# Optimization experiments

Measured on AMD Instinct MI355X. Metric: run time of the kernel, lower is better.

## Reference

```python
import jax, jax.numpy as jnp
import numpy as np

B, C, H, W = 4, 256, 64, 64
CQ = C // 8


def setup_inputs() -> dict:
    key = jax.random.key(0)
    ks = jax.random.split(key, 7)
    x = jax.random.normal(ks[0], (B, C, H, W), dtype=jnp.float32)
    Wq = jax.random.normal(ks[1], (CQ, C), dtype=jnp.float32) * 0.02
    bq = jnp.zeros((CQ,), dtype=jnp.float32)
    Wk = jax.random.normal(ks[2], (CQ, C), dtype=jnp.float32) * 0.02
    bk = jnp.zeros((CQ,), dtype=jnp.float32)
    Wv = jax.random.normal(ks[3], (C, C), dtype=jnp.float32) * 0.02
    bv = jnp.zeros((C,), dtype=jnp.float32)
    return {"x": x, "Wq": Wq, "bq": bq, "Wk": Wk, "bk": bk, "Wv": Wv, "bv": bv}


def reference(x, Wq, bq, Wk, bk, Wv, bv):
    b, c, h, w = x.shape
    n = h * w
    xf = x.reshape(b, c, n)                                   # [B,C,N]
    # 1x1 convs are per-pixel GEMMs
    q = jnp.einsum('qc,bcn->bnq', Wq, xf) + bq                # [B,N,Cq]
    k = jnp.einsum('qc,bcn->bqn', Wk, xf) + bk[None, :, None] # [B,Cq,N]
    v = jnp.einsum('vc,bcn->bnv', Wv, xf) + bv                # [B,N,C]
    scale = float(n) ** 0.5
    energy = jnp.einsum('bnq,bqm->bnm', q, k) / scale         # [B,N,N]
    attn = jax.nn.softmax(energy, axis=-1)
    out = jnp.einsum('bnm,bmv->bnv', attn, v)                 # [B,N,C]
    # Faithful to torch's out.view(B,C,H,W) applied to the contiguous [B,N,C]
    # tensor: a raw memory reinterpretation, NOT a transpose.
    return out.reshape(b, c, h, w)
```

## Files before the change

### kernel.cpp

```cpp
#include <hip/hip_runtime.h>

#define BATCH 4
#define CH    256
#define NPIX  4096
#define CQD   32

typedef __bf16 bf16;
typedef bf16 bf16x8 __attribute__((ext_vector_type(8)));
typedef bf16 bf16x4 __attribute__((ext_vector_type(4)));
typedef float f32x4 __attribute__((ext_vector_type(4)));
typedef float f32x16 __attribute__((ext_vector_type(16)));

#define MFMA16 __builtin_amdgcn_mfma_f32_16x16x32_bf16
#define MFMA32 __builtin_amdgcn_mfma_f32_32x32x16_bf16

#define GLOAD_LDS16(g, l) __builtin_amdgcn_global_load_lds( \
    (const __attribute__((address_space(1))) void*)(g),     \
    (__attribute__((address_space(3))) void*)(l), 16, 0, 0)

__device__ __forceinline__ float fast_exp2(float x) {
#if __has_builtin(__builtin_amdgcn_exp2f)
    return __builtin_amdgcn_exp2f(x);
#else
    return __expf(x * 0.69314718055994530942f);
#endif
}

#define QSCALE (0.015625f * 1.44269504088896340736f)

__global__ __launch_bounds__(256) void prep_kernel(
    const float* __restrict__ Wq, const float* __restrict__ bq,
    const float* __restrict__ Wk, const float* __restrict__ bk,
    const float* __restrict__ Wv, const float* __restrict__ bv,
    bf16* __restrict__ Wb, float* __restrict__ bb)
{
    int r = blockIdx.x, c = threadIdx.x;
    const float* W; const float* bs; float sc; int rr;
    if (r < 32)      { W = Wq; bs = bq; sc = QSCALE; rr = r; }
    else if (r < 64) { W = Wk; bs = bk; sc = 1.0f;   rr = r - 32; }
    else             { W = Wv; bs = bv; sc = 1.0f;   rr = r - 64; }
    Wb[(size_t)r * CH + c] = (bf16)(W[(size_t)rr * CH + c] * sc);
    if (c == 0) bb[r] = bs[rr] * sc;
}

__global__ __launch_bounds__(256) void proj_kernel(
    const float* __restrict__ x,
    const bf16* __restrict__ Wb, const float* __restrict__ bb,
    bf16* __restrict__ qp, bf16* __restrict__ kp, bf16* __restrict__ vT)
{
    __shared__ __align__(16) bf16 xT[32][264];
    __shared__ __align__(16) bf16 vstage[4][16][40];

    const int t  = threadIdx.x;
    const int b  = blockIdx.x >> 7;
    const int n0 = (blockIdx.x & 127) << 5;
    const int w    = t >> 6;
    const int lane = t & 63;
    const int l16  = t & 15;
    const int quad = (t & 63) >> 4;

    const float* xb = x + (size_t)b * CH * NPIX;
#pragma unroll
    for (int j = 0; j < 8; ++j) {
        int id = t + j * 256;
        int c  = id >> 3;
        int n4 = (id & 7) << 2;
        float4 vv = *(const float4*)(xb + (size_t)c * NPIX + n0 + n4);
        xT[n4 + 0][c] = (bf16)vv.x;
        xT[n4 + 1][c] = (bf16)vv.y;
        xT[n4 + 2][c] = (bf16)vv.z;
        xT[n4 + 3][c] = (bf16)vv.w;
    }
    __syncthreads();

    for (int rt = 0; rt < 5; ++rt) {
        int ro = w * 80 + rt * 16;
        int kind = (ro < 32) ? 0 : (ro < 64) ? 1 : 2;

        bf16x8 afrag[8];
        const bf16* wrow = Wb + (size_t)(ro + l16) * CH + quad * 8;
#pragma unroll
        for (int kc = 0; kc < 8; ++kc)
            afrag[kc] = *(const bf16x8*)(wrow + kc * 32);
        float bv4[4];
#pragma unroll
        for (int r = 0; r < 4; ++r) bv4[r] = bb[ro + quad * 4 + r];

#pragma unroll
        for (int nt = 0; nt < 2; ++nt) {
            f32x4 acc = {0.f, 0.f, 0.f, 0.f};
#pragma unroll
            for (int kc = 0; kc < 8; ++kc) {
                bf16x8 bfr = *(const bf16x8*)&xT[nt * 16 + l16][kc * 32 + quad * 8];
                acc = MFMA16(afrag[kc], bfr, acc, 0, 0, 0);
            }
            if (kind != 2) {
                bf16x4 pk;
#pragma unroll
                for (int r = 0; r < 4; ++r)
                    pk[r] = (bf16)(acc[r] + bv4[r]);
                int n = n0 + nt * 16 + l16;
                int col = (kind == 0 ? ro : ro - 32) + quad * 4;
                bf16* dst = (kind == 0) ? qp : kp;
                *(bf16x4*)&dst[((size_t)b * NPIX + n) * CQD + col] = pk;
            } else {
#pragma unroll
                for (int r = 0; r < 4; ++r)
                    vstage[w][quad * 4 + r][nt * 16 + l16] = (bf16)(acc[r] + bv4[r]);
            }
        }
        if (kind == 2) {
            int vrow = lane >> 2, vcc = lane & 3;
            bf16x8 chunk = *(const bf16x8*)&vstage[w][vrow][vcc * 8];
            *(bf16x8*)&vT[((size_t)b * CH + (ro - 64) + vrow) * NPIX + n0 + vcc * 8] = chunk;
        }
    }
}

template<int S, bool DIRECT>
__global__ __launch_bounds__(256, 2) void attn_kernel(
    const bf16* __restrict__ qp, const bf16* __restrict__ kp,
    const bf16* __restrict__ vT,
    bf16* __restrict__ Opart, float* __restrict__ Lpart,
    float* __restrict__ out)
{
    __shared__ __align__(16) bf16 Vt[2][256][64];
    __shared__ __align__(16) bf16 PbS[128][64];

    const int t    = threadIdx.x;
    const int bid  = blockIdx.x;
    const int s    = bid % S;
    const int tq   = bid / S;
    const int b    = tq >> 5;
    const int qt   = tq & 31;
    const int n0   = qt << 7;
    const int w    = t >> 6;
    const int lane = t & 63;
    const int l16  = t & 15;
    const int quad = (t & 63) >> 4;
    const int sw   = l16 & 7;
    const int l32  = lane & 31;
    const int h    = lane >> 5;
    const int qh   = w >> 1;
    const int chb  = (w & 1) * 128;

    const bf16* qpb = qp + ((size_t)b * NPIX + n0 + w * 32) * CQD;
    bf16x8 qfrag[2];
    qfrag[0] = *(const bf16x8*)(qpb + (size_t)l16 * CQD + quad * 8);
    qfrag[1] = *(const bf16x8*)(qpb + (size_t)(16 + l16) * CQD + quad * 8);

    f32x16 o[2][4];
#pragma unroll
    for (int i = 0; i < 2; ++i)
#pragma unroll
        for (int j = 0; j < 4; ++j)
#pragma unroll
            for (int r = 0; r < 16; ++r) o[i][j][r] = 0.f;
    float lsum[2] = {0.f, 0.f};

    const bf16* kpb = kp + (size_t)b * NPIX * CQD;
    const bf16* vTb = vT + (size_t)b * CH * NPIX;
    const int k0 = s * (NPIX / S);
    const int iters = NPIX / S / 64;

    const int vrow_off = lane >> 3;
    const int vchunk   = (lane & 7) ^ vrow_off;
    auto issue_vt = [&](int buf, int m0) {
#pragma unroll
        for (int j = 0; j < 8; ++j) {
            int rowbase = j * 32 + w * 8;
            const bf16* src = vTb + (size_t)(rowbase + vrow_off) * NPIX + m0 + vchunk * 8;
            GLOAD_LDS16(src, &Vt[buf][rowbase][0]);
        }
    };
    auto load_kf = [&](int m0, bf16x8* kf) {
#pragma unroll
        for (int mt = 0; mt < 4; ++mt)
            kf[mt] = *(const bf16x8*)(kpb + (size_t)(m0 + mt * 16 + l16) * CQD + quad * 8);
    };

    bf16x8 kfa[4], kfb[4];
    issue_vt(0, k0);
    load_kf(k0, kfa);
    __syncthreads();

    for (int mi = 0; mi < iters; ++mi) {
        const int cur = mi & 1;
        const int m0  = k0 + (mi << 6);
        if (mi + 1 < iters) {
            issue_vt(cur ^ 1, m0 + 64);
            load_kf(m0 + 64, kfb);
        }

        f32x4 sv[2][4];
#pragma unroll
        for (int mt = 0; mt < 4; ++mt) {
            f32x4 z = {0.f, 0.f, 0.f, 0.f};
            sv[0][mt] = MFMA16(kfa[mt], qfrag[0], z, 0, 0, 0);
            sv[1][mt] = MFMA16(kfa[mt], qfrag[1], z, 0, 0, 0);
        }

#pragma unroll
        for (int g = 0; g < 2; ++g) {
            float rs = 0.f;
#pragma unroll
            for (int mt = 0; mt < 4; ++mt) {
                bf16x4 pk;
#pragma unroll
                for (int r = 0; r < 4; ++r) {
                    float e = fast_exp2(sv[g][mt][r]);
                    rs += e;
                    pk[r] = (bf16)e;
                }
                int slot = (2 * mt + (quad >> 1)) ^ sw;
                *(bf16x4*)&PbS[w * 32 + g * 16 + l16][slot * 8 + (quad & 1) * 4] = pk;
            }
            lsum[g] += rs;
        }
        __syncthreads();

        bf16x8 pA[2][4];
#pragma unroll
        for (int t32 = 0; t32 < 2; ++t32)
#pragma unroll
            for (int kg = 0; kg < 4; ++kg) {
                int row = qh * 64 + t32 * 32 + l32;
                pA[t32][kg] = *(const bf16x8*)&PbS[row][((2 * kg + h) ^ (l32 & 7)) * 8];
            }
#pragma unroll
        for (int ct = 0; ct < 4; ++ct) {
            int vrow = chb + ct * 32 + l32;
            bf16x8 vB[4];
#pragma unroll
            for (int kg = 0; kg < 4; ++kg)
                vB[kg] = *(const bf16x8*)&Vt[cur][vrow][((2 * kg + h) ^ (l32 & 7)) * 8];
#pragma unroll
            for (int t32 = 0; t32 < 2; ++t32)
#pragma unroll
                for (int kg = 0; kg < 4; ++kg)
                    o[t32][ct] = MFMA32(pA[t32][kg], vB[kg], o[t32][ct], 0, 0, 0);
        }
        __syncthreads();
#pragma unroll
        for (int i = 0; i < 4; ++i) kfa[i] = kfb[i];
    }

    float l_g[2];
#pragma unroll
    for (int g = 0; g < 2; ++g) {
        float v = lsum[g];
        v += __shfl_xor(v, 16);
        v += __shfl_xor(v, 32);
        l_g[g] = v;
    }
    float* lsh = (float*)PbS;
    if (quad == 0) {
#pragma unroll
        for (int g = 0; g < 2; ++g)
            lsh[w * 32 + g * 16 + l16] = l_g[g];
    }
    __syncthreads();

    const size_t prb2 = ((size_t)s * BATCH + b) * NPIX + n0;
    if (!DIRECT && quad == 0) {
#pragma unroll
        for (int g = 0; g < 2; ++g)
            Lpart[prb2 + w * 32 + g * 16 + l16] = l_g[g];
    }

    bf16* eb = (bf16*)Vt + (size_t)w * 32 * 136;
#pragma unroll
    for (int t32 = 0; t32 < 2; ++t32) {
        float rinv[16];
#pragma unroll
        for (int reg = 0; reg < 16; ++reg) {
            int q_r = (reg & 3) + 8 * (reg >> 2) + 4 * h;
            rinv[reg] = 1.0f / lsh[qh * 64 + t32 * 32 + q_r];
        }
        if (!DIRECT) {
#pragma unroll
            for (int ct = 0; ct < 4; ++ct)
#pragma unroll
                for (int reg = 0; reg < 16; ++reg) {
                    int q_r = (reg & 3) + 8 * (reg >> 2) + 4 * h;
                    eb[q_r * 136 + ct * 32 + l32] = (bf16)(o[t32][ct][reg] * rinv[reg]);
                }
            int vrow = lane >> 4, vcc = lane & 15;
#pragma unroll
            for (int p = 0; p < 8; ++p) {
                int row = p * 4 + vrow;
                bf16x8 chunk = *(const bf16x8*)&eb[row * 136 + vcc * 8];
                *(bf16x8*)&Opart[(prb2 + qh * 64 + t32 * 32 + row) * CH +
                                 chb + vcc * 8] = chunk;
            }
        } else {
            float* ob = out + (prb2 + qh * 64 + t32 * 32) * CH + chb;
#pragma unroll
            for (int ct = 0; ct < 4; ++ct)
#pragma unroll
                for (int reg = 0; reg < 16; ++reg) {
                    int q_r = (reg & 3) + 8 * (reg >> 2) + 4 * h;
                    ob[(size_t)q_r * CH + ct * 32 + l32] = o[t32][ct][reg] * rinv[reg];
                }
        }
    }
}

template<int S>
__global__ __launch_bounds__(256) void combine_kernel(
    const bf16* __restrict__ Opart, const float* __restrict__ Lpart,
    float* __restrict__ out)
{
    int idx  = blockIdx.x * 256 + threadIdx.x;
    int nrow = idx >> 4;
    int cc   = (idx & 15) * 16;
    int b    = nrow >> 12, nin = nrow & 4095;

    size_t pr[S];
    float  ls[S], wsum = 0.f;
#pragma unroll
    for (int s = 0; s < S; ++s) {
        pr[s] = ((size_t)s * BATCH + b) * NPIX + nin;
        ls[s] = Lpart[pr[s]];
        wsum += ls[s];
    }
    float inv = 1.0f / wsum;

    bf16x8 ov[S][2];
#pragma unroll
    for (int s = 0; s < S; ++s) {
        ov[s][0] = *(const bf16x8*)&Opart[pr[s] * CH + cc];
        ov[s][1] = *(const bf16x8*)&Opart[pr[s] * CH + cc + 8];
    }

    float acc[16];
#pragma unroll
    for (int j = 0; j < 16; ++j) acc[j] = 0.f;
#pragma unroll
    for (int s = 0; s < S; ++s) {
        float wn = ls[s] * inv;
#pragma unroll
        for (int k = 0; k < 2; ++k)
#pragma unroll
            for (int j = 0; j < 8; ++j)
                acc[k * 8 + j] += wn * (float)ov[s][k][j];
    }
#pragma unroll
    for (int k = 0; k < 4; ++k) {
        float4 o4 = {acc[4 * k], acc[4 * k + 1], acc[4 * k + 2], acc[4 * k + 3]};
        *(float4*)&out[(size_t)nrow * CH + cc + 4 * k] = o4;
    }
}

extern "C" void kernel_launch(void* const* d_in, const int* in_sizes, int n_in,
                              void* d_out, int out_size, void* d_ws, size_t ws_size,
                              hipStream_t stream) {
    const float* x  = (const float*)d_in[0];
    const float* Wq = (const float*)d_in[1];
    const float* bq = (const float*)d_in[2];
    const float* Wk = (const float*)d_in[3];
    const float* bk = (const float*)d_in[4];
    const float* Wv = (const float*)d_in[5];
    const float* bv = (const float*)d_in[6];
    float* out = (float*)d_out;

    char* ws = (char*)d_ws;
    const size_t qpB   = (size_t)BATCH * NPIX * CQD * 2;
    const size_t vTB   = (size_t)BATCH * CH * NPIX * 2;
    const size_t WbB   = (size_t)320 * CH * 2;
    const size_t bbB   = 320 * 4 + 768;
    const size_t baseB = 2 * qpB + vTB + WbB + bbB;
    const size_t oprtB = (size_t)BATCH * NPIX * CH * 2;
    const size_t mlB   = (size_t)BATCH * NPIX * 4;

    bf16*  qp = (bf16*)ws;
    bf16*  kp = (bf16*)(ws + qpB);
    bf16*  vT = (bf16*)(ws + 2 * qpB);
    bf16*  Wb = (bf16*)(ws + 2 * qpB + vTB);
    float* bb = (float*)(ws + 2 * qpB + vTB + WbB);

    prep_kernel<<<dim3(320), dim3(256), 0, stream>>>(Wq, bq, Wk, bk, Wv, bv, Wb, bb);
    proj_kernel<<<dim3(BATCH * (NPIX / 32)), dim3(256), 0, stream>>>(
        x, Wb, bb, qp, kp, vT);

    auto need = [&](int S) { return baseB + (size_t)S * (oprtB + mlB); };
    int S = (ws_size >= need(4)) ? 4 : (ws_size >= need(2)) ? 2
          : (ws_size >= need(1)) ? 1 : 0;

    if (S > 0) {
        bf16*  Opart = (bf16*)(ws + baseB);
        float* Lpart = (float*)(ws + baseB + (size_t)S * oprtB);
        if (S == 4) {
            attn_kernel<4, false><<<dim3(128 * 4), dim3(256), 0, stream>>>(
                qp, kp, vT, Opart, Lpart, out);
            combine_kernel<4><<<dim3(1024), dim3(256), 0, stream>>>(Opart, Lpart, out);
        } else if (S == 2) {
            attn_kernel<2, false><<<dim3(128 * 2), dim3(256), 0, stream>>>(
                qp, kp, vT, Opart, Lpart, out);
            combine_kernel<2><<<dim3(1024), dim3(256), 0, stream>>>(Opart, Lpart, out);
        } else {
            attn_kernel<1, false><<<dim3(128), dim3(256), 0, stream>>>(
                qp, kp, vT, Opart, Lpart, out);
            combine_kernel<1><<<dim3(1024), dim3(256), 0, stream>>>(Opart, Lpart, out);
        }
    } else {
        attn_kernel<1, true><<<dim3(128), dim3(256), 0, stream>>>(
            qp, kp, vT, nullptr, nullptr, out);
    }
}
```

Baseline: 142.7 us.

## Give each wave its own query rows for PV to drop block barrier

The PV stage changes so each wave multiplies only its own 32 query rows of P against all 256 value channels. Previously each wave took 64 rows by 128 channels, which read P rows written by other waves. Because each wave now consumes only the P rows it produced, the block-wide barrier between softmax and PV is removed, and the final row-sum exchange uses per-wave LDS with a waitcnt instead of a barrier. In exchange every wave now reads all 256 Vt rows from LDS, doubling V LDS traffic, and holds 8 f32x16 accumulators at the same register count.

```diff
diff --git a/kernel.cpp b/kernel.cpp
--- a/kernel.cpp
+++ b/kernel.cpp
@@ -141,21 +141,17 @@
     const int sw   = l16 & 7;
     const int l32  = lane & 31;
     const int h    = lane >> 5;
-    const int qh   = w >> 1;
-    const int chb  = (w & 1) * 128;
 
     const bf16* qpb = qp + ((size_t)b * NPIX + n0 + w * 32) * CQD;
     bf16x8 qfrag[2];
     qfrag[0] = *(const bf16x8*)(qpb + (size_t)l16 * CQD + quad * 8);
     qfrag[1] = *(const bf16x8*)(qpb + (size_t)(16 + l16) * CQD + quad * 8);
 
-    f32x16 o[2][4];
-#pragma unroll
-    for (int i = 0; i < 2; ++i)
-#pragma unroll
-        for (int j = 0; j < 4; ++j)
-#pragma unroll
-            for (int r = 0; r < 16; ++r) o[i][j][r] = 0.f;
+    f32x16 o[8];
+#pragma unroll
+    for (int j = 0; j < 8; ++j)
+#pragma unroll
+        for (int r = 0; r < 16; ++r) o[j][r] = 0.f;
     float lsum[2] = {0.f, 0.f};
 
     const bf16* kpb = kp + (size_t)b * NPIX * CQD;
@@ -217,28 +213,21 @@
             }
             lsum[g] += rs;
         }
-        __syncthreads();
-
-        bf16x8 pA[2][4];
-#pragma unroll
-        for (int t32 = 0; t32 < 2; ++t32)
-#pragma unroll
-            for (int kg = 0; kg < 4; ++kg) {
-                int row = qh * 64 + t32 * 32 + l32;
-                pA[t32][kg] = *(const bf16x8*)&PbS[row][((2 * kg + h) ^ (l32 & 7)) * 8];
-            }
-#pragma unroll
-        for (int ct = 0; ct < 4; ++ct) {
-            int vrow = chb + ct * 32 + l32;
+
+        bf16x8 pA[4];
+#pragma unroll
+        for (int kg = 0; kg < 4; ++kg)
+            pA[kg] = *(const bf16x8*)&PbS[w * 32 + l32][((2 * kg + h) ^ (l32 & 7)) * 8];
+#pragma unroll
+        for (int ct = 0; ct < 8; ++ct) {
+            int vrow = ct * 32 + l32;
             bf16x8 vB[4];
 #pragma unroll
             for (int kg = 0; kg < 4; ++kg)
                 vB[kg] = *(const bf16x8*)&Vt[cur][vrow][((2 * kg + h) ^ (l32 & 7)) * 8];
 #pragma unroll
-            for (int t32 = 0; t32 < 2; ++t32)
-#pragma unroll
-                for (int kg = 0; kg < 4; ++kg)
-                    o[t32][ct] = MFMA32(pA[t32][kg], vB[kg], o[t32][ct], 0, 0, 0);
+            for (int kg = 0; kg < 4; ++kg)
+                o[ct] = MFMA32(pA[kg], vB[kg], o[ct], 0, 0, 0);
         }
         __syncthreads();
 #pragma unroll
@@ -253,13 +242,13 @@
         v += __shfl_xor(v, 32);
         l_g[g] = v;
     }
-    float* lsh = (float*)PbS;
+    float* lshw = (float*)((char*)PbS + (size_t)w * 4096);
     if (quad == 0) {
 #pragma unroll
         for (int g = 0; g < 2; ++g)
-            lsh[w * 32 + g * 16 + l16] = l_g[g];
-    }
-    __syncthreads();
+            lshw[g * 16 + l16] = l_g[g];
+    }
+    __builtin_amdgcn_s_waitcnt(0);
 
     const size_t prb2 = ((size_t)s * BATCH + b) * NPIX + n0;
     if (!DIRECT && quad == 0) {
@@ -268,41 +257,42 @@
             Lpart[prb2 + w * 32 + g * 16 + l16] = l_g[g];
     }
 
-    bf16* eb = (bf16*)Vt + (size_t)w * 32 * 136;
-#pragma unroll
-    for (int t32 = 0; t32 < 2; ++t32) {
-        float rinv[16];
-#pragma unroll
-        for (int reg = 0; reg < 16; ++reg) {
-            int q_r = (reg & 3) + 8 * (reg >> 2) + 4 * h;
-            rinv[reg] = 1.0f / lsh[qh * 64 + t32 * 32 + q_r];
-        }
-        if (!DIRECT) {
+    float rinv[16];
+#pragma unroll
+    for (int reg = 0; reg < 16; ++reg) {
+        int q_r = (reg & 3) + 8 * (reg >> 2) + 4 * h;
+        rinv[reg] = 1.0f / lshw[q_r];
+    }
+    if (!DIRECT) {
+        bf16* eb = (bf16*)Vt + (size_t)w * 32 * 136;
+#pragma unroll
+        for (int p2 = 0; p2 < 2; ++p2) {
 #pragma unroll
             for (int ct = 0; ct < 4; ++ct)
 #pragma unroll
                 for (int reg = 0; reg < 16; ++reg) {
                     int q_r = (reg & 3) + 8 * (reg >> 2) + 4 * h;
-                    eb[q_r * 136 + ct * 32 + l32] = (bf16)(o[t32][ct][reg] * rinv[reg]);
+                    eb[q_r * 136 + ct * 32 + l32] =
+                        (bf16)(o[p2 * 4 + ct][reg] * rinv[reg]);
                 }
             int vrow = lane >> 4, vcc = lane & 15;
 #pragma unroll
             for (int p = 0; p < 8; ++p) {
                 int row = p * 4 + vrow;
                 bf16x8 chunk = *(const bf16x8*)&eb[row * 136 + vcc * 8];
-                *(bf16x8*)&Opart[(prb2 + qh * 64 + t32 * 32 + row) * CH +
-                                 chb + vcc * 8] = chunk;
+                *(bf16x8*)&Opart[(prb2 + w * 32 + row) * CH +
+                                 p2 * 128 + vcc * 8] = chunk;
             }
-        } else {
-            float* ob = out + (prb2 + qh * 64 + t32 * 32) * CH + chb;
-#pragma unroll
-            for (int ct = 0; ct < 4; ++ct)
-#pragma unroll
-                for (int reg = 0; reg < 16; ++reg) {
-                    int q_r = (reg & 3) + 8 * (reg >> 2) + 4 * h;
-                    ob[(size_t)q_r * CH + ct * 32 + l32] = o[t32][ct][reg] * rinv[reg];
-                }
-        }
+        }
+    } else {
+        float* ob = out + (prb2 + w * 32) * CH;
+#pragma unroll
+        for (int ct = 0; ct < 8; ++ct)
+#pragma unroll
+            for (int reg = 0; reg < 16; ++reg) {
+                int q_r = (reg & 3) + 8 * (reg >> 2) + 4 * h;
+                ob[(size_t)q_r * CH + ct * 32 + l32] = o[ct][reg] * rinv[reg];
+            }
     }
 }
 
```

After: 144.9 us. No clear change (+1.5%).
